# Kernel optimization log

Measured on AMD Instinct MI355X. Metric: run time of the kernel, lower is better.

Reference implementation:

```python
import jax, jax.numpy as jnp
import numpy as np

NUM_LEVELS = 3
NUM_STEPS = 4
STEP_SIZE = 2.0
MAX_ITER = 10
MOMENTUM = 0.1
D2R = np.array([np.pi / 180] * 3 + [1.0] * 3, dtype=np.float32)  # (6,) degree->rad for angles


def _rotmat(a):
    # a: (3,) rotation angles in radians; R = Rz @ Ry @ Rx
    cx, sx = jnp.cos(a[0]), jnp.sin(a[0])
    cy, sy = jnp.cos(a[1]), jnp.sin(a[1])
    cz, sz = jnp.cos(a[2]), jnp.sin(a[2])
    one = jnp.ones((), a.dtype)
    zero = jnp.zeros((), a.dtype)
    Rx = jnp.stack([jnp.stack([one, zero, zero]), jnp.stack([zero, cx, -sx]), jnp.stack([zero, sx, cx])])
    Ry = jnp.stack([jnp.stack([cy, zero, sy]), jnp.stack([zero, one, zero]), jnp.stack([-sy, zero, cy])])
    Rz = jnp.stack([jnp.stack([cz, -sz, zero]), jnp.stack([sz, cz, zero]), jnp.stack([zero, zero, one])])
    return Rz @ Ry @ Rx


def _warp_one(theta_deg, vol):
    # theta_deg: (6,) [rx,ry,rz in degrees, tx,ty,tz in normalized coords]; vol: (D,D,D)
    ang = theta_deg[:3] * jnp.float32(np.pi / 180)
    t = theta_deg[3:]
    R = _rotmat(ang)
    D = vol.shape[0]
    lin = jnp.linspace(-1.0, 1.0, D, dtype=vol.dtype)
    g0, g1, g2 = jnp.meshgrid(lin, lin, lin, indexing='ij')
    pts = jnp.stack([g0.ravel(), g1.ravel(), g2.ravel()])  # (3, D^3)
    p = R @ pts + t[:, None]
    idx = (p + 1.0) * ((D - 1) / 2.0)  # normalized [-1,1] -> voxel coords
    out = jax.scipy.ndimage.map_coordinates(vol, [idx[0], idx[1], idx[2]], order=1, mode='constant', cval=0.0)
    return out.reshape(D, D, D)


def _evaluate(theta_deg, src, tgt):
    # src/tgt: (B,1,D,D,D) -> per-sample mean MSE (loss(...).view(B,-1).mean(1))
    warped = jax.vmap(_warp_one)(theta_deg, src[:, 0])
    diff = (warped - tgt[:, 0]) ** 2
    return diff.reshape(diff.shape[0], -1).mean(1)


def _pool(x, f):
    # update_level: 2^level average-pool pyramid
    if f == 1:
        return x
    B, C, D = x.shape[0], x.shape[1], x.shape[2]
    return x.reshape(B, C, D // f, f, D // f, f, D // f, f).mean(axis=(3, 5, 7))


def _run_level(theta_deg, src, tgt, step_size0):
    # singlelevel(): num_steps outer steps, step_size halved each step,
    # each step runs max_iter masked GD iterations with FD gradients.
    B = theta_deg.shape[0]
    eye = jnp.eye(6, dtype=theta_deg.dtype)
    signed = jnp.concatenate([eye, -eye], axis=0)  # (12,6): +e_j rows then -e_j rows
    ev = lambda th: _evaluate(th, src, tgt)
    ev_fd = jax.vmap(ev)  # over the 12 FD perturbations

    buf = jnp.zeros_like(theta_deg)          # momentum buffer (created lazily in torch)
    has_buf = jnp.zeros((), bool)
    loss_all = jnp.zeros((B,), theta_deg.dtype)
    ss = step_size0
    for _ in range(NUM_STEPS):
        def body(i, state, ss=ss):
            theta, active, loss_all, buf, has_buf = state
            loss = ev(theta)
            lf = ev_fd(theta[None, :, :] + ss * signed[:, None, :])  # (12,B)
            grad = (lf[:6] - lf[6:]).T  # (B,6) undivided central differences (as in torch)
            loss_all = jnp.where(active, loss, loss_all)
            # gd_step with momentum: buf=grad on first call, else buf[active]=buf[active]*m+grad
            upd = jnp.where(has_buf, buf * MOMENTUM + grad, grad)
            buf = jnp.where(active[:, None], upd, buf)
            has_buf = jnp.ones((), bool)
            d = buf / (jnp.linalg.norm(buf, axis=-1, keepdims=True) + 1e-6)
            theta_try = theta + (-ss) * d
            loss_new = ev(theta_try)
            new_active = active & ((loss_new + 1e-4) < loss)  # shrinking active set
            theta = jnp.where(new_active[:, None], theta_try, theta)
            return theta, new_active, loss_all, buf, has_buf
        active = jnp.ones((B,), bool)
        theta_deg, active, loss_all, buf, has_buf = jax.lax.fori_loop(
            0, MAX_ITER, body, (theta_deg, active, loss_all, buf, has_buf))
        ss = ss / 2.0
    return theta_deg, loss_all


def _forward(theta, source, target):
    d2r = jnp.asarray(D2R)
    theta0 = theta
    # rad2degree(theta.detach())
    theta_deg = jax.lax.stop_gradient(theta / d2r)
    loss = jnp.zeros((theta.shape[0],), theta.dtype)
    for level in range(NUM_LEVELS - 1, -1, -1):
        f = 2 ** level
        theta_deg, loss = _run_level(theta_deg, _pool(source, f), _pool(target, f), STEP_SIZE * (2 ** level))
    # dtheta computed under no_grad; out = theta0 + dtheta
    dtheta = jax.lax.stop_gradient(theta_deg * d2r - theta0)
    return theta0 + dtheta, jax.lax.stop_gradient(loss)


def setup_inputs() -> dict:
    key = jax.random.key(0)
    k1, k2, k3 = jax.random.split(key, 3)
    B, D = 8, 64
    theta = jax.random.normal(k1, (B, 6), dtype=jnp.float32) * 0.05  # small initial misalignment (radians / normalized)
    source = jax.random.uniform(k2, (B, 1, D, D, D), dtype=jnp.float32)
    target = jax.random.uniform(k3, (B, 1, D, D, D), dtype=jnp.float32)
    return {"theta": theta, "source": source, "target": target}


def reference(theta, source, target):
    return _forward(theta, source, target)
```

## Files before the change

### kernel.cpp

```cpp
#include <hip/hip_runtime.h>

#define PI180F 0.017453292519943295f

__device__ __forceinline__ void compute_R(const float th[6], float R[9], float t[3]) {
    float ax = th[0] * PI180F, ay = th[1] * PI180F, az = th[2] * PI180F;
    float cx = cosf(ax), sx = sinf(ax);
    float cy = cosf(ay), sy = sinf(ay);
    float cz = cosf(az), sz = sinf(az);
    R[0] = cz * cy;  R[1] = (cz * sy) * sx - sz * cx;  R[2] = (cz * sy) * cx + sz * sx;
    R[3] = sz * cy;  R[4] = (sz * sy) * sx + cz * cx;  R[5] = (sz * sy) * cx - cz * sx;
    R[6] = -sy;      R[7] = cy * sx;                   R[8] = cy * cx;
    t[0] = th[3]; t[1] = th[4]; t[2] = th[5];
}

template<int D>
__device__ __forceinline__ float tri_sample_pad(const float* __restrict__ vol,
                                                float c0, float c1, float c2) {
    constexpr int P = D + 3;
    float f0 = floorf(c0), f1 = floorf(c1), f2 = floorf(c2);
    int i0 = (int)f0, i1 = (int)f1, i2 = (int)f2;
    float t0 = c0 - f0, t1 = c1 - f1, t2 = c2 - f2;
    float w0[2] = {1.0f - t0, t0};
    float w1[2] = {1.0f - t1, t1};
    float w2[2] = {1.0f - t2, t2};
    int ip0 = ((unsigned)(i0 + 1) <= (unsigned)D) ? (i0 + 1) : (D + 1);
    int ip1 = ((unsigned)(i1 + 1) <= (unsigned)D) ? (i1 + 1) : (D + 1);
    int ip2 = ((unsigned)(i2 + 1) <= (unsigned)D) ? (i2 + 1) : (D + 1);
    const float* p = vol + ((ip0 * P + ip1) * P + ip2);
    float acc = 0.0f;
    acc += ((w0[0] * w1[0]) * w2[0]) * p[0];
    acc += ((w0[0] * w1[0]) * w2[1]) * p[1];
    acc += ((w0[0] * w1[1]) * w2[0]) * p[P];
    acc += ((w0[0] * w1[1]) * w2[1]) * p[P + 1];
    acc += ((w0[1] * w1[0]) * w2[0]) * p[P * P];
    acc += ((w0[1] * w1[0]) * w2[1]) * p[P * P + 1];
    acc += ((w0[1] * w1[1]) * w2[0]) * p[P * P + P];
    acc += ((w0[1] * w1[1]) * w2[1]) * p[P * P + P + 1];
    return acc;
}

template<int D, int K>
__device__ __forceinline__ void eval_block(
    const float* __restrict__ srcp, const float* __restrict__ tgt,
    const float th[6], int b, int k, double* __restrict__ red)
{
    constexpr int logD = (D == 64) ? 6 : ((D == 32) ? 5 : 4);
    constexpr int n = D * D * D;
    constexpr int PS = (D + 3) * (D + 3) * (D + 3);
    float R[9], t[3];
    compute_R(th, R, t);

    constexpr int chunk = n / K;
    const int vstart = k * chunk;
    const float step = 2.0f / (float)(D - 1);
    const float scale = (float)(D - 1) * 0.5f;
    const float* s = srcp + (size_t)b * PS;
    const float* g = tgt + (size_t)b * n;

    double acc = 0.0;
    for (int v = vstart + threadIdx.x; v < vstart + chunk; v += 256) {
        int kk = v & (D - 1);
        int jj = (v >> logD) & (D - 1);
        int ii = v >> (2 * logD);
        float x0 = -1.0f + (float)ii * step;
        float x1 = -1.0f + (float)jj * step;
        float x2 = -1.0f + (float)kk * step;
        float p0 = R[0] * x0 + R[1] * x1 + R[2] * x2 + t[0];
        float p1 = R[3] * x0 + R[4] * x1 + R[5] * x2 + t[1];
        float p2 = R[6] * x0 + R[7] * x1 + R[8] * x2 + t[2];
        float c0 = (p0 + 1.0f) * scale;
        float c1 = (p1 + 1.0f) * scale;
        float c2 = (p2 + 1.0f) * scale;
        float w = tri_sample_pad<D>(s, c0, c1, c2);
        float d = w - g[v];
        acc += (double)(d * d);
    }

    red[threadIdx.x] = acc;
    __syncthreads();
#pragma unroll
    for (int st = 128; st > 0; st >>= 1) {
        if (threadIdx.x < st) red[threadIdx.x] += red[threadIdx.x + st];
        __syncthreads();
    }
}

template<int D, int K>
__global__ __launch_bounds__(256) void fd_kernel(
    const float* __restrict__ srcp, const float* __restrict__ tgt,
    const float* __restrict__ thetaIn, const float* __restrict__ lcurIn,
    const int* __restrict__ activeIn,
    float* __restrict__ thetaOut, float* __restrict__ lcurOut,
    int* __restrict__ activeOut,
    const float* __restrict__ ttry, const double* __restrict__ pB,
    double* __restrict__ partials,
    float ss, int first, int apply, int reset, int k3prev, int nprev)
{
    __shared__ double red[256];
    __shared__ float sth[6];
    __shared__ int sact;
    const int tid = threadIdx.x;
    const int gb = blockIdx.x;
    const int k = gb % K;
    const int e = gb / K;
    const int b = e & 7;
    const int c = first ? (e >> 3) : (e >> 3) + 1;

    if (apply) {
        if (tid < 32) {
            double v = (tid < k3prev) ? pB[b * k3prev + tid] : 0.0;
            v += __shfl_down(v, 16, 32);
            v += __shfl_down(v, 8, 32);
            v += __shfl_down(v, 4, 32);
            v += __shfl_down(v, 2, 32);
            v += __shfl_down(v, 1, 32);
            if (tid == 0) {
                int na = activeIn[b];
                float l = lcurIn[b];
                float th[6];
#pragma unroll
                for (int j = 0; j < 6; ++j) th[j] = thetaIn[b * 6 + j];
                if (na) {
                    float ln = (float)(v / (double)nprev);
                    if (ln + 1e-4f < l) {
#pragma unroll
                        for (int j = 0; j < 6; ++j) th[j] = ttry[b * 6 + j];
                        l = ln;
                    } else {
                        na = 0;
                    }
                }
                if (reset) na = 1;
#pragma unroll
                for (int j = 0; j < 6; ++j) sth[j] = th[j];
                sact = na;
                if (((e >> 3) == 0) && (k == 0)) {
#pragma unroll
                    for (int j = 0; j < 6; ++j) thetaOut[b * 6 + j] = th[j];
                    lcurOut[b] = l;
                    activeOut[b] = na;
                }
            }
        }
        __syncthreads();
    } else {
        if (tid < 6) sth[tid] = thetaIn[b * 6 + tid];
        if (tid == 0) sact = activeIn[b];
        __syncthreads();
    }

    if (!sact) return;
    float th[6];
#pragma unroll
    for (int j = 0; j < 6; ++j) th[j] = sth[j];
    if (c > 0) {
        int j = (c - 1) % 6;
        th[j] += (c <= 6) ? ss : -ss;
    }
    eval_block<D, K>(srcp, tgt, th, b, k, red);
    if (tid == 0) partials[(size_t)(c * 8 + b) * K + k] = red[0];
}

template<int D, int K3, int K>
__global__ __launch_bounds__(256) void trial_kernel(
    const float* __restrict__ srcp, const float* __restrict__ tgt,
    const float* __restrict__ theta, float* __restrict__ lcur,
    const int* __restrict__ active,
    const float* __restrict__ momIn, float* __restrict__ momOut,
    float* __restrict__ ttry, float* __restrict__ lall,
    const double* __restrict__ pA, double* __restrict__ pB,
    float ss, int first)
{
    constexpr int n = D * D * D;
    __shared__ double red[256];
    __shared__ float lossf[13];
    __shared__ float sttry[6];
    const int tid = threadIdx.x;
    const int gb = blockIdx.x;
    const int k = gb % K3;
    const int b = gb / K3;

    if (!active[b]) {
        if (k == 0 && tid < 6) momOut[b * 6 + tid] = momIn[b * 6 + tid];
        return;
    }

    const int nconf = first ? 13 : 12;
#pragma unroll
    for (int p = 0; p < 2; ++p) {
        int ci = p * 8 + (tid >> 5);
        if (ci < nconf) {
            int ca = first ? ci : ci + 1;
            int kk = tid & 31;
            double v = (kk < K) ? pA[(size_t)(ca * 8 + b) * K + kk] : 0.0;
            v += __shfl_down(v, 16, 32);
            v += __shfl_down(v, 8, 32);
            v += __shfl_down(v, 4, 32);
            v += __shfl_down(v, 2, 32);
            v += __shfl_down(v, 1, 32);
            if (kk == 0) lossf[ca] = (float)(v / (double)n);
        }
    }
    __syncthreads();
    if (tid == 0) {
        float lb = first ? lossf[0] : lcur[b];
        float ub[6];
#pragma unroll
        for (int j = 0; j < 6; ++j) {
            float grad = lossf[1 + j] - lossf[7 + j];
            float u = first ? grad : (momIn[b * 6 + j] * 0.1f + grad);
            ub[j] = u;
        }
        float ss2 = 0.0f;
#pragma unroll
        for (int j = 0; j < 6; ++j) ss2 += ub[j] * ub[j];
        float denom = sqrtf(ss2) + 1e-6f;
#pragma unroll
        for (int j = 0; j < 6; ++j) sttry[j] = theta[b * 6 + j] - ss * (ub[j] / denom);
        if (k == 0) {
            lall[b] = lb;
            if (first) lcur[b] = lb;
#pragma unroll
            for (int j = 0; j < 6; ++j) momOut[b * 6 + j] = ub[j];
#pragma unroll
            for (int j = 0; j < 6; ++j) ttry[b * 6 + j] = sttry[j];
        }
    }
    __syncthreads();
    float th[6];
#pragma unroll
    for (int j = 0; j < 6; ++j) th[j] = sttry[j];
    eval_block<D, K3>(srcp, tgt, th, b, k, red);
    if (tid == 0) pB[(size_t)b * K3 + k] = red[0];
}

__global__ __launch_bounds__(256) void finalize_kernel(
    const float* __restrict__ theta0,
    const float* __restrict__ theta, const float* __restrict__ lcur,
    const int* __restrict__ active, const float* __restrict__ ttry,
    const double* __restrict__ pB, const float* __restrict__ lall,
    float* __restrict__ out)
{
    __shared__ double rs[8];
    __shared__ float fth[48];
    const int tid = threadIdx.x;
    const int r = tid >> 5, l = tid & 31;
    {
        double v = pB[r * 32 + l];
        v += __shfl_down(v, 16, 32);
        v += __shfl_down(v, 8, 32);
        v += __shfl_down(v, 4, 32);
        v += __shfl_down(v, 2, 32);
        v += __shfl_down(v, 1, 32);
        if (l == 0) rs[r] = v;
    }
    __syncthreads();
    if (tid < 8) {
        int b = tid;
        bool acc = false;
        if (active[b]) {
            float ln = (float)(rs[b] / 262144.0);
            acc = (ln + 1e-4f < lcur[b]);
        }
        for (int j = 0; j < 6; ++j)
            fth[b * 6 + j] = acc ? ttry[b * 6 + j] : theta[b * 6 + j];
    }
    __syncthreads();
    if (tid < 48) {
        int j = tid % 6;
        float d2r = (j < 3) ? PI180F : 1.0f;
        float td = fth[tid] * d2r;
        out[tid] = theta0[tid] + (td - theta0[tid]);
    } else if (tid < 56) {
        out[tid] = lall[tid - 48];
    }
}

template<int f>
__global__ void pool_pad_kernel(const float* __restrict__ src, const float* __restrict__ tgt,
                                float* __restrict__ srcp, float* __restrict__ tgtp)
{
    constexpr int Do = 64 / f;
    constexpr int P = Do + 3;
    constexpr int n = 8 * Do * Do * Do;
    int idx = blockIdx.x * blockDim.x + threadIdx.x;
    if (idx >= 2 * n) return;
    bool is_src = idx < n;
    int id = is_src ? idx : idx - n;
    int kk = id % Do;
    int jj = (id / Do) % Do;
    int ii = (id / (Do * Do)) % Do;
    int b  = id / (Do * Do * Do);
    const float* v = (is_src ? src : tgt) + (size_t)b * 262144;
    double s = 0.0;
    for (int p = 0; p < f; ++p)
        for (int q = 0; q < f; ++q)
            for (int r = 0; r < f; ++r)
                s += (double)v[((ii * f + p) * 64 + (jj * f + q)) * 64 + (kk * f + r)];
    float val = (float)(s / (double)(f * f * f));
    if (is_src) srcp[(size_t)b * P * P * P + (((ii + 1) * P + (jj + 1)) * P + (kk + 1))] = val;
    else        tgtp[id] = val;
}

__global__ void pad_copy_kernel(const float* __restrict__ src, float* __restrict__ dst)
{
    int idx = blockIdx.x * blockDim.x + threadIdx.x;
    if (idx >= 8 * 262144) return;
    int kk = idx & 63;
    int jj = (idx >> 6) & 63;
    int ii = (idx >> 12) & 63;
    int b  = idx >> 18;
    dst[(size_t)b * 67 * 67 * 67 + (((ii + 1) * 67 + (jj + 1)) * 67 + (kk + 1))] = src[idx];
}

__global__ void init_kernel(const float* __restrict__ theta_in,
                            float* __restrict__ theta_deg,
                            float* __restrict__ lcur,
                            int* __restrict__ active)
{
    int t = threadIdx.x;
    if (t < 48) {
        int j = t % 6;
        float d2r = (j < 3) ? PI180F : 1.0f;
        theta_deg[t] = theta_in[t] / d2r;
    }
    if (t < 8) { active[t] = 1; lcur[t] = 0.0f; }
}

template<int D, int K, int K3>
static void run_level(const float* srcp, const float* tgt,
                      float* const thetaS[2], float* const lcurS[2], int* const activeS[2],
                      float* const momS[2], float* ttry, float* lall,
                      double* pA, double* pB,
                      int L, int& scur, int& mcur, int k3prevLvl, int nprevLvl,
                      float ss0, hipStream_t stream)
{
    float ssv = ss0;
    for (int s = 0; s < 4; ++s) {
        for (int it = 0; it < 10; ++it) {
            int first = (s == 0 && it == 0) ? 1 : 0;
            int apply = !(L == 0 && first);
            int reset = (it == 0) ? 1 : 0;
            int k3p = first ? k3prevLvl : K3;
            int np  = first ? nprevLvl  : D * D * D;
            int nconf = first ? 13 : 12;
            int so = apply ? (scur ^ 1) : scur;
            fd_kernel<D, K><<<nconf * 8 * K, 256, 0, stream>>>(
                srcp, tgt,
                thetaS[scur], lcurS[scur], activeS[scur],
                thetaS[so], lcurS[so], activeS[so],
                ttry, pB, pA, ssv, first, apply, reset, k3p, np);
            if (apply) scur ^= 1;
            trial_kernel<D, K3, K><<<8 * K3, 256, 0, stream>>>(
                srcp, tgt,
                thetaS[scur], lcurS[scur], activeS[scur],
                momS[mcur], momS[mcur ^ 1], ttry, lall, pA, pB, ssv, first);
            mcur ^= 1;
        }
        ssv *= 0.5f;
    }
}

extern "C" void kernel_launch(void* const* d_in, const int* in_sizes, int n_in,
                              void* d_out, int out_size, void* d_ws, size_t ws_size,
                              hipStream_t stream)
{
    const float* theta0 = (const float*)d_in[0];
    const float* source = (const float*)d_in[1];
    const float* target = (const float*)d_in[2];
    float* out = (float*)d_out;

    char* ws = (char*)d_ws;
    size_t off = 0;
    auto alloc = [&](size_t bytes) -> void* {
        off = (off + 255) & ~(size_t)255;
        void* p = ws + off;
        off += bytes;
        return p;
    };
    float* thetaS[2] = { (float*)alloc(48 * 4), (float*)alloc(48 * 4) };
    float* lcurS[2]  = { (float*)alloc(8 * 4),  (float*)alloc(8 * 4)  };
    int*   activeS[2]= { (int*)alloc(8 * 4),    (int*)alloc(8 * 4)    };
    float* momS[2]   = { (float*)alloc(48 * 4), (float*)alloc(48 * 4) };
    float* ttry  = (float*)alloc(48 * 4);
    float* lall  = (float*)alloc(8 * 4);
    double* pA   = (double*)alloc(13 * 8 * 32 * 8);
    double* pB   = (double*)alloc(8 * 32 * 8);
    float* tgt2  = (float*)alloc((size_t)8 * 32768 * 4);
    float* tgt4  = (float*)alloc((size_t)8 * 4096 * 4);
    const size_t PS16 = 19 * 19 * 19, PS32 = 35 * 35 * 35, PS64 = 67 * 67 * 67;
    float* pad16 = (float*)alloc((size_t)8 * PS16 * 4);
    float* pad32 = (float*)alloc((size_t)8 * PS32 * 4);
    float* pad64 = (float*)alloc((size_t)8 * PS64 * 4);

    hipMemsetAsync(pad16, 0, (size_t)8 * PS16 * 4, stream);
    hipMemsetAsync(pad32, 0, (size_t)8 * PS32 * 4, stream);
    hipMemsetAsync(pad64, 0, (size_t)8 * PS64 * 4, stream);

    pool_pad_kernel<2><<<(2 * 8 * 32768 + 255) / 256, 256, 0, stream>>>(source, target, pad32, tgt2);
    pool_pad_kernel<4><<<(2 * 8 * 4096 + 255) / 256, 256, 0, stream>>>(source, target, pad16, tgt4);
    pad_copy_kernel<<<(8 * 262144 + 255) / 256, 256, 0, stream>>>(source, pad64);
    init_kernel<<<1, 64, 0, stream>>>(theta0, thetaS[0], lcurS[0], activeS[0]);

    int scur = 0, mcur = 0;
    run_level<16,  2, 16>(pad16, tgt4,   thetaS, lcurS, activeS, momS, ttry, lall,
                          pA, pB, 0, scur, mcur, 16, 4096, 8.0f, stream);
    run_level<32,  8, 32>(pad32, tgt2,   thetaS, lcurS, activeS, momS, ttry, lall,
                          pA, pB, 1, scur, mcur, 16, 4096, 4.0f, stream);
    run_level<64, 32, 32>(pad64, target, thetaS, lcurS, activeS, momS, ttry, lall,
                          pA, pB, 2, scur, mcur, 32, 32768, 2.0f, stream);

    finalize_kernel<<<1, 256, 0, stream>>>(
        theta0, thetaS[scur], lcurS[scur], activeS[scur], ttry, pB, lall, out);
}
```

Measured before the change: 963.8 us.

## Restructure voxel loop by rows and raise trial split for level 64

The evaluation loop now assigns 16-thread groups to rows of the output grid. Each group computes the row-invariant part of the rotated coordinates once and reuses it across the row, which removes per-voxel index decoding and some multiply-adds. The level-64 trial kernel is split into 128 blocks per sample instead of 32, to use more of the GPU. The partial-sum reductions in the fd and finalize kernels now loop to handle more than 32 partials. Launch bounds now request 4 blocks per SM, which may limit registers and cause spills.

```diff
diff --git a/kernel.cpp b/kernel.cpp
--- a/kernel.cpp
+++ b/kernel.cpp
@@ -47,33 +47,48 @@
     constexpr int logD = (D == 64) ? 6 : ((D == 32) ? 5 : 4);
     constexpr int n = D * D * D;
     constexpr int PS = (D + 3) * (D + 3) * (D + 3);
+    constexpr int chunk = n / K;
+    constexpr int ROWS = chunk / D;
+    constexpr int NS = D / 16;
+    const float step = 2.0f / (float)(D - 1);
+    const float scale = (float)(D - 1) * 0.5f;
+
     float R[9], t[3];
     compute_R(th, R, t);
 
-    constexpr int chunk = n / K;
-    const int vstart = k * chunk;
-    const float step = 2.0f / (float)(D - 1);
-    const float scale = (float)(D - 1) * 0.5f;
     const float* s = srcp + (size_t)b * PS;
     const float* g = tgt + (size_t)b * n;
 
+    const int l15 = threadIdx.x & 15;
+    const int grp = threadIdx.x >> 4;
+    const int row0 = k * ROWS;
+
     double acc = 0.0;
-    for (int v = vstart + threadIdx.x; v < vstart + chunk; v += 256) {
-        int kk = v & (D - 1);
-        int jj = (v >> logD) & (D - 1);
-        int ii = v >> (2 * logD);
+#pragma unroll 2
+    for (int rit = 0; rit < ROWS / 16; ++rit) {
+        int row = row0 + rit * 16 + grp;
+        int ii = row >> logD;
+        int jj = row & (D - 1);
         float x0 = -1.0f + (float)ii * step;
         float x1 = -1.0f + (float)jj * step;
-        float x2 = -1.0f + (float)kk * step;
-        float p0 = R[0] * x0 + R[1] * x1 + R[2] * x2 + t[0];
-        float p1 = R[3] * x0 + R[4] * x1 + R[5] * x2 + t[1];
-        float p2 = R[6] * x0 + R[7] * x1 + R[8] * x2 + t[2];
-        float c0 = (p0 + 1.0f) * scale;
-        float c1 = (p1 + 1.0f) * scale;
-        float c2 = (p2 + 1.0f) * scale;
-        float w = tri_sample_pad<D>(s, c0, c1, c2);
-        float d = w - g[v];
-        acc += (double)(d * d);
+        float A0 = R[0] * x0 + R[1] * x1;
+        float A1 = R[3] * x0 + R[4] * x1;
+        float A2 = R[6] * x0 + R[7] * x1;
+        const float* grow = g + row * D;
+#pragma unroll
+        for (int si = 0; si < NS; ++si) {
+            int kk = l15 + si * 16;
+            float x2 = -1.0f + (float)kk * step;
+            float p0 = A0 + R[2] * x2 + t[0];
+            float p1 = A1 + R[5] * x2 + t[1];
+            float p2 = A2 + R[8] * x2 + t[2];
+            float c0 = (p0 + 1.0f) * scale;
+            float c1 = (p1 + 1.0f) * scale;
+            float c2 = (p2 + 1.0f) * scale;
+            float w = tri_sample_pad<D>(s, c0, c1, c2);
+            float d = w - grow[kk];
+            acc += (double)(d * d);
+        }
     }
 
     red[threadIdx.x] = acc;
@@ -86,7 +101,7 @@
 }
 
 template<int D, int K>
-__global__ __launch_bounds__(256) void fd_kernel(
+__global__ __launch_bounds__(256, 4) void fd_kernel(
     const float* __restrict__ srcp, const float* __restrict__ tgt,
     const float* __restrict__ thetaIn, const float* __restrict__ lcurIn,
     const int* __restrict__ activeIn,
@@ -108,7 +123,8 @@
 
     if (apply) {
         if (tid < 32) {
-            double v = (tid < k3prev) ? pB[b * k3prev + tid] : 0.0;
+            double v = 0.0;
+            for (int i = tid; i < k3prev; i += 32) v += pB[b * k3prev + i];
             v += __shfl_down(v, 16, 32);
             v += __shfl_down(v, 8, 32);
             v += __shfl_down(v, 4, 32);
@@ -162,7 +178,7 @@
 }
 
 template<int D, int K3, int K>
-__global__ __launch_bounds__(256) void trial_kernel(
+__global__ __launch_bounds__(256, 4) void trial_kernel(
     const float* __restrict__ srcp, const float* __restrict__ tgt,
     const float* __restrict__ theta, float* __restrict__ lcur,
     const int* __restrict__ active,
@@ -246,7 +262,8 @@
     const int tid = threadIdx.x;
     const int r = tid >> 5, l = tid & 31;
     {
-        double v = pB[r * 32 + l];
+        double v = 0.0;
+        for (int i = l; i < 128; i += 32) v += pB[r * 128 + i];
         v += __shfl_down(v, 16, 32);
         v += __shfl_down(v, 8, 32);
         v += __shfl_down(v, 4, 32);
@@ -385,7 +402,7 @@
     float* ttry  = (float*)alloc(48 * 4);
     float* lall  = (float*)alloc(8 * 4);
     double* pA   = (double*)alloc(13 * 8 * 32 * 8);
-    double* pB   = (double*)alloc(8 * 32 * 8);
+    double* pB   = (double*)alloc(8 * 128 * 8);
     float* tgt2  = (float*)alloc((size_t)8 * 32768 * 4);
     float* tgt4  = (float*)alloc((size_t)8 * 4096 * 4);
     const size_t PS16 = 19 * 19 * 19, PS32 = 35 * 35 * 35, PS64 = 67 * 67 * 67;
@@ -403,12 +420,12 @@
     init_kernel<<<1, 64, 0, stream>>>(theta0, thetaS[0], lcurS[0], activeS[0]);
 
     int scur = 0, mcur = 0;
-    run_level<16,  2, 16>(pad16, tgt4,   thetaS, lcurS, activeS, momS, ttry, lall,
-                          pA, pB, 0, scur, mcur, 16, 4096, 8.0f, stream);
-    run_level<32,  8, 32>(pad32, tgt2,   thetaS, lcurS, activeS, momS, ttry, lall,
-                          pA, pB, 1, scur, mcur, 16, 4096, 4.0f, stream);
-    run_level<64, 32, 32>(pad64, target, thetaS, lcurS, activeS, momS, ttry, lall,
-                          pA, pB, 2, scur, mcur, 32, 32768, 2.0f, stream);
+    run_level<16,  2,  16>(pad16, tgt4,   thetaS, lcurS, activeS, momS, ttry, lall,
+                           pA, pB, 0, scur, mcur, 16, 4096, 8.0f, stream);
+    run_level<32,  8,  32>(pad32, tgt2,   thetaS, lcurS, activeS, momS, ttry, lall,
+                           pA, pB, 1, scur, mcur, 16, 4096, 4.0f, stream);
+    run_level<64, 32, 128>(pad64, target, thetaS, lcurS, activeS, momS, ttry, lall,
+                           pA, pB, 2, scur, mcur, 32, 32768, 2.0f, stream);
 
     finalize_kernel<<<1, 256, 0, stream>>>(
         theta0, thetaS[scur], lcurS[scur], activeS[scur], ttry, pB, lall, out);
```

Result: slower. 1.005 ms (+4.2%).

## Fuse trial evaluation with next iteration's FD evaluation into one kernel

Applied to the files above, without the earlier changes.

Merges the separate finite-difference kernel and trial-step kernel into a single opt_kernel. Each launch now decides on the previous trial, computes the next trial point, and evaluates the 12 perturbed losses around it, plus the trial point itself as configuration 0. This roughly halves the number of dependent launches per iteration and removes their launch and serialization gaps. It also changes K per level, folds padding zero-fill into the pooling and copy kernels in place of the memsets, and double-buffers ttry and the partials. The cost is extra evaluations around a trial that may get rejected, and more complex state handling.

```diff
diff --git a/kernel.cpp b/kernel.cpp
--- a/kernel.cpp
+++ b/kernel.cpp
@@ -1,6 +1,11 @@
 #include <hip/hip_runtime.h>
 
 #define PI180F 0.017453292519943295f
+
+#define F_APPLY  1
+#define F_RESET  2
+#define F_UPD    4
+#define F_BASEC0 8
 
 __device__ __forceinline__ void compute_R(const float th[6], float R[9], float t[3]) {
     float ax = th[0] * PI180F, ay = th[1] * PI180F, az = th[2] * PI180F;
@@ -52,13 +57,14 @@
 
     constexpr int chunk = n / K;
     const int vstart = k * chunk;
+    const int vend = vstart + chunk;
     const float step = 2.0f / (float)(D - 1);
     const float scale = (float)(D - 1) * 0.5f;
     const float* s = srcp + (size_t)b * PS;
     const float* g = tgt + (size_t)b * n;
 
     double acc = 0.0;
-    for (int v = vstart + threadIdx.x; v < vstart + chunk; v += 256) {
+    for (int v = vstart + threadIdx.x; v < vend; v += 256) {
         int kk = v & (D - 1);
         int jj = (v >> logD) & (D - 1);
         int ii = v >> (2 * logD);
@@ -86,29 +92,38 @@
 }
 
 template<int D, int K>
-__global__ __launch_bounds__(256) void fd_kernel(
+__global__ __launch_bounds__(256) void opt_kernel(
     const float* __restrict__ srcp, const float* __restrict__ tgt,
     const float* __restrict__ thetaIn, const float* __restrict__ lcurIn,
     const int* __restrict__ activeIn,
     float* __restrict__ thetaOut, float* __restrict__ lcurOut,
     int* __restrict__ activeOut,
-    const float* __restrict__ ttry, const double* __restrict__ pB,
-    double* __restrict__ partials,
-    float ss, int first, int apply, int reset, int k3prev, int nprev)
-{
+    float* __restrict__ lcurW,
+    const float* __restrict__ momIn, float* __restrict__ momOut,
+    const float* __restrict__ ttryIn, float* __restrict__ ttryOut,
+    float* __restrict__ lall,
+    const double* __restrict__ pIn, double* __restrict__ pOut,
+    float ss, int cbase, int flags, int k3prev, int nprev)
+{
+    constexpr int n = D * D * D;
     __shared__ double red[256];
-    __shared__ float sth[6];
+    __shared__ float lossf[13];
+    __shared__ float sth[6], sttry[6];
+    __shared__ float slcur;
     __shared__ int sact;
+
     const int tid = threadIdx.x;
     const int gb = blockIdx.x;
     const int k = gb % K;
     const int e = gb / K;
     const int b = e & 7;
-    const int c = first ? (e >> 3) : (e >> 3) + 1;
-
-    if (apply) {
+    const int c = cbase + (e >> 3);
+    const bool desig = ((e >> 3) == 0) && (k == 0);
+
+    if (flags & F_APPLY) {
         if (tid < 32) {
-            double v = (tid < k3prev) ? pB[b * k3prev + tid] : 0.0;
+            double v = 0.0;
+            for (int i = tid; i < k3prev; i += 32) v += pIn[b * k3prev + i];
             v += __shfl_down(v, 16, 32);
             v += __shfl_down(v, 8, 32);
             v += __shfl_down(v, 4, 32);
@@ -124,17 +139,18 @@
                     float ln = (float)(v / (double)nprev);
                     if (ln + 1e-4f < l) {
 #pragma unroll
-                        for (int j = 0; j < 6; ++j) th[j] = ttry[b * 6 + j];
+                        for (int j = 0; j < 6; ++j) th[j] = ttryIn[b * 6 + j];
                         l = ln;
                     } else {
                         na = 0;
                     }
                 }
-                if (reset) na = 1;
+                if (flags & F_RESET) na = 1;
 #pragma unroll
                 for (int j = 0; j < 6; ++j) sth[j] = th[j];
                 sact = na;
-                if (((e >> 3) == 0) && (k == 0)) {
+                slcur = l;
+                if (desig) {
 #pragma unroll
                     for (int j = 0; j < 6; ++j) thetaOut[b * 6 + j] = th[j];
                     lcurOut[b] = l;
@@ -142,96 +158,74 @@
                 }
             }
         }
-        __syncthreads();
     } else {
         if (tid < 6) sth[tid] = thetaIn[b * 6 + tid];
-        if (tid == 0) sact = activeIn[b];
+        if (tid == 0) { sact = activeIn[b]; slcur = lcurIn[b]; }
+    }
+    __syncthreads();
+
+    if (flags & F_UPD) {
+        if (sact) {
+            const bool bc0 = (flags & F_BASEC0) != 0;
+            const int nsl = bc0 ? 13 : 12;
+#pragma unroll
+            for (int p = 0; p < 2; ++p) {
+                int ci = p * 8 + (tid >> 5);
+                if (ci < nsl) {
+                    int ca = bc0 ? ci : ci + 1;
+                    int kk = tid & 31;
+                    double v = 0.0;
+                    for (int i = kk; i < K; i += 32) v += pIn[(size_t)(ca * 8 + b) * K + i];
+                    v += __shfl_down(v, 16, 32);
+                    v += __shfl_down(v, 8, 32);
+                    v += __shfl_down(v, 4, 32);
+                    v += __shfl_down(v, 2, 32);
+                    v += __shfl_down(v, 1, 32);
+                    if (kk == 0) lossf[ca] = (float)(v / (double)n);
+                }
+            }
+            __syncthreads();
+            if (tid == 0) {
+                float lb = bc0 ? lossf[0] : slcur;
+                float ub[6];
+#pragma unroll
+                for (int j = 0; j < 6; ++j) {
+                    float grad = lossf[1 + j] - lossf[7 + j];
+                    float u = bc0 ? grad : (momIn[b * 6 + j] * 0.1f + grad);
+                    ub[j] = u;
+                }
+                float ss2 = 0.0f;
+#pragma unroll
+                for (int j = 0; j < 6; ++j) ss2 += ub[j] * ub[j];
+                float denom = sqrtf(ss2) + 1e-6f;
+#pragma unroll
+                for (int j = 0; j < 6; ++j) sttry[j] = sth[j] - ss * (ub[j] / denom);
+                if (desig) {
+                    lall[b] = lb;
+                    if (bc0) lcurW[b] = lb;
+#pragma unroll
+                    for (int j = 0; j < 6; ++j) momOut[b * 6 + j] = ub[j];
+#pragma unroll
+                    for (int j = 0; j < 6; ++j) ttryOut[b * 6 + j] = sttry[j];
+                }
+            }
+        } else {
+            if (desig && tid < 6) momOut[b * 6 + tid] = momIn[b * 6 + tid];
+        }
         __syncthreads();
     }
 
     if (!sact) return;
-    float th[6];
-#pragma unroll
-    for (int j = 0; j < 6; ++j) th[j] = sth[j];
+
+    float evth[6];
+#pragma unroll
+    for (int j = 0; j < 6; ++j) evth[j] = (flags & F_UPD) ? sttry[j] : sth[j];
     if (c > 0) {
         int j = (c - 1) % 6;
-        th[j] += (c <= 6) ? ss : -ss;
-    }
-    eval_block<D, K>(srcp, tgt, th, b, k, red);
-    if (tid == 0) partials[(size_t)(c * 8 + b) * K + k] = red[0];
-}
-
-template<int D, int K3, int K>
-__global__ __launch_bounds__(256) void trial_kernel(
-    const float* __restrict__ srcp, const float* __restrict__ tgt,
-    const float* __restrict__ theta, float* __restrict__ lcur,
-    const int* __restrict__ active,
-    const float* __restrict__ momIn, float* __restrict__ momOut,
-    float* __restrict__ ttry, float* __restrict__ lall,
-    const double* __restrict__ pA, double* __restrict__ pB,
-    float ss, int first)
-{
-    constexpr int n = D * D * D;
-    __shared__ double red[256];
-    __shared__ float lossf[13];
-    __shared__ float sttry[6];
-    const int tid = threadIdx.x;
-    const int gb = blockIdx.x;
-    const int k = gb % K3;
-    const int b = gb / K3;
-
-    if (!active[b]) {
-        if (k == 0 && tid < 6) momOut[b * 6 + tid] = momIn[b * 6 + tid];
-        return;
-    }
-
-    const int nconf = first ? 13 : 12;
-#pragma unroll
-    for (int p = 0; p < 2; ++p) {
-        int ci = p * 8 + (tid >> 5);
-        if (ci < nconf) {
-            int ca = first ? ci : ci + 1;
-            int kk = tid & 31;
-            double v = (kk < K) ? pA[(size_t)(ca * 8 + b) * K + kk] : 0.0;
-            v += __shfl_down(v, 16, 32);
-            v += __shfl_down(v, 8, 32);
-            v += __shfl_down(v, 4, 32);
-            v += __shfl_down(v, 2, 32);
-            v += __shfl_down(v, 1, 32);
-            if (kk == 0) lossf[ca] = (float)(v / (double)n);
-        }
-    }
-    __syncthreads();
-    if (tid == 0) {
-        float lb = first ? lossf[0] : lcur[b];
-        float ub[6];
-#pragma unroll
-        for (int j = 0; j < 6; ++j) {
-            float grad = lossf[1 + j] - lossf[7 + j];
-            float u = first ? grad : (momIn[b * 6 + j] * 0.1f + grad);
-            ub[j] = u;
-        }
-        float ss2 = 0.0f;
-#pragma unroll
-        for (int j = 0; j < 6; ++j) ss2 += ub[j] * ub[j];
-        float denom = sqrtf(ss2) + 1e-6f;
-#pragma unroll
-        for (int j = 0; j < 6; ++j) sttry[j] = theta[b * 6 + j] - ss * (ub[j] / denom);
-        if (k == 0) {
-            lall[b] = lb;
-            if (first) lcur[b] = lb;
-#pragma unroll
-            for (int j = 0; j < 6; ++j) momOut[b * 6 + j] = ub[j];
-#pragma unroll
-            for (int j = 0; j < 6; ++j) ttry[b * 6 + j] = sttry[j];
-        }
-    }
-    __syncthreads();
-    float th[6];
-#pragma unroll
-    for (int j = 0; j < 6; ++j) th[j] = sttry[j];
-    eval_block<D, K3>(srcp, tgt, th, b, k, red);
-    if (tid == 0) pB[(size_t)b * K3 + k] = red[0];
+        evth[j] += (c <= 6) ? ss : -ss;
+    }
+    eval_block<D, K>(srcp, tgt, evth, b, k, red);
+    if (tid == 0) pOut[(size_t)(c * 8 + b) * K + k] = red[0];
 }
 
 __global__ __launch_bounds__(256) void finalize_kernel(
@@ -282,35 +276,54 @@
 {
     constexpr int Do = 64 / f;
     constexpr int P = Do + 3;
-    constexpr int n = 8 * Do * Do * Do;
+    constexpr int nPad = 8 * P * P * P;
+    constexpr int nLin = 8 * Do * Do * Do;
     int idx = blockIdx.x * blockDim.x + threadIdx.x;
-    if (idx >= 2 * n) return;
-    bool is_src = idx < n;
-    int id = is_src ? idx : idx - n;
-    int kk = id % Do;
-    int jj = (id / Do) % Do;
-    int ii = (id / (Do * Do)) % Do;
-    int b  = id / (Do * Do * Do);
-    const float* v = (is_src ? src : tgt) + (size_t)b * 262144;
-    double s = 0.0;
-    for (int p = 0; p < f; ++p)
-        for (int q = 0; q < f; ++q)
-            for (int r = 0; r < f; ++r)
-                s += (double)v[((ii * f + p) * 64 + (jj * f + q)) * 64 + (kk * f + r)];
-    float val = (float)(s / (double)(f * f * f));
-    if (is_src) srcp[(size_t)b * P * P * P + (((ii + 1) * P + (jj + 1)) * P + (kk + 1))] = val;
-    else        tgtp[id] = val;
+    if (idx < nPad) {
+        int kk = idx % P;
+        int jj = (idx / P) % P;
+        int ii = (idx / (P * P)) % P;
+        int b  = idx / (P * P * P);
+        float val = 0.0f;
+        if (ii >= 1 && ii <= Do && jj >= 1 && jj <= Do && kk >= 1 && kk <= Do) {
+            const float* v = src + (size_t)b * 262144;
+            int i0 = ii - 1, j0 = jj - 1, k0 = kk - 1;
+            double s = 0.0;
+            for (int p = 0; p < f; ++p)
+                for (int q = 0; q < f; ++q)
+                    for (int r = 0; r < f; ++r)
+                        s += (double)v[((i0 * f + p) * 64 + (j0 * f + q)) * 64 + (k0 * f + r)];
+            val = (float)(s / (double)(f * f * f));
+        }
+        srcp[idx] = val;
+    } else if (idx < nPad + nLin) {
+        int id = idx - nPad;
+        int kk = id % Do;
+        int jj = (id / Do) % Do;
+        int ii = (id / (Do * Do)) % Do;
+        int b  = id / (Do * Do * Do);
+        const float* v = tgt + (size_t)b * 262144;
+        double s = 0.0;
+        for (int p = 0; p < f; ++p)
+            for (int q = 0; q < f; ++q)
+                for (int r = 0; r < f; ++r)
+                    s += (double)v[((ii * f + p) * 64 + (jj * f + q)) * 64 + (kk * f + r)];
+        tgtp[id] = (float)(s / (double)(f * f * f));
+    }
 }
 
 __global__ void pad_copy_kernel(const float* __restrict__ src, float* __restrict__ dst)
 {
     int idx = blockIdx.x * blockDim.x + threadIdx.x;
-    if (idx >= 8 * 262144) return;
-    int kk = idx & 63;
-    int jj = (idx >> 6) & 63;
-    int ii = (idx >> 12) & 63;
-    int b  = idx >> 18;
-    dst[(size_t)b * 67 * 67 * 67 + (((ii + 1) * 67 + (jj + 1)) * 67 + (kk + 1))] = src[idx];
+    if (idx >= 8 * 67 * 67 * 67) return;
+    int kk = idx % 67;
+    int jj = (idx / 67) % 67;
+    int ii = (idx / (67 * 67)) % 67;
+    int b  = idx / (67 * 67 * 67);
+    float v = 0.0f;
+    if (ii >= 1 && ii <= 64 && jj >= 1 && jj <= 64 && kk >= 1 && kk <= 64)
+        v = src[(((size_t)b * 64 + (ii - 1)) * 64 + (jj - 1)) * 64 + (kk - 1)];
+    dst[idx] = v;
 }
 
 __global__ void init_kernel(const float* __restrict__ theta_in,
@@ -327,35 +340,54 @@
     if (t < 8) { active[t] = 1; lcur[t] = 0.0f; }
 }
 
-template<int D, int K, int K3>
-static void run_level(const float* srcp, const float* tgt,
-                      float* const thetaS[2], float* const lcurS[2], int* const activeS[2],
-                      float* const momS[2], float* ttry, float* lall,
-                      double* pA, double* pB,
-                      int L, int& scur, int& mcur, int k3prevLvl, int nprevLvl,
-                      float ss0, hipStream_t stream)
-{
+struct Bufs {
+    float *thetaS[2], *lcurS[2], *momS[2], *ttryS[2];
+    int   *activeS[2];
+    float *lall;
+    double *P[2];
+};
+
+template<int D, int K>
+static void run_level(const float* srcp, const float* tgt, Bufs& bf,
+                      int& scur, int& mcur, int& tcur, int& pcur,
+                      int k3prevLvl, int nprevLvl, float ss0, bool veryFirst,
+                      hipStream_t stream)
+{
+    constexpr int n = D * D * D;
     float ssv = ss0;
     for (int s = 0; s < 4; ++s) {
-        for (int it = 0; it < 10; ++it) {
-            int first = (s == 0 && it == 0) ? 1 : 0;
-            int apply = !(L == 0 && first);
-            int reset = (it == 0) ? 1 : 0;
-            int k3p = first ? k3prevLvl : K3;
-            int np  = first ? nprevLvl  : D * D * D;
-            int nconf = first ? 13 : 12;
-            int so = apply ? (scur ^ 1) : scur;
-            fd_kernel<D, K><<<nconf * 8 * K, 256, 0, stream>>>(
+        {
+            int flags = F_RESET | ((veryFirst && s == 0) ? 0 : F_APPLY);
+            int cb    = (s == 0) ? 0 : 1;
+            int nconf = (s == 0) ? 13 : 12;
+            int k3p   = (s == 0) ? k3prevLvl : K;
+            int np    = (s == 0) ? nprevLvl  : n;
+            opt_kernel<D, K><<<nconf * 8 * K, 256, 0, stream>>>(
                 srcp, tgt,
-                thetaS[scur], lcurS[scur], activeS[scur],
-                thetaS[so], lcurS[so], activeS[so],
-                ttry, pB, pA, ssv, first, apply, reset, k3p, np);
-            if (apply) scur ^= 1;
-            trial_kernel<D, K3, K><<<8 * K3, 256, 0, stream>>>(
+                bf.thetaS[scur], bf.lcurS[scur], bf.activeS[scur],
+                bf.thetaS[scur ^ 1], bf.lcurS[scur ^ 1], bf.activeS[scur ^ 1],
+                bf.lcurS[scur],
+                bf.momS[mcur], bf.momS[mcur ^ 1],
+                bf.ttryS[tcur], bf.ttryS[tcur ^ 1],
+                bf.lall, bf.P[pcur], bf.P[pcur ^ 1],
+                ssv, cb, flags, k3p, np);
+            if (flags & F_APPLY) scur ^= 1;
+            pcur ^= 1;
+        }
+        for (int j = 1; j <= 10; ++j) {
+            int flags = F_UPD | ((j == 1) ? ((s == 0) ? F_BASEC0 : 0) : F_APPLY);
+            int nconf = (j == 10) ? 1 : 13;
+            opt_kernel<D, K><<<nconf * 8 * K, 256, 0, stream>>>(
                 srcp, tgt,
-                thetaS[scur], lcurS[scur], activeS[scur],
-                momS[mcur], momS[mcur ^ 1], ttry, lall, pA, pB, ssv, first);
-            mcur ^= 1;
+                bf.thetaS[scur], bf.lcurS[scur], bf.activeS[scur],
+                bf.thetaS[scur ^ 1], bf.lcurS[scur ^ 1], bf.activeS[scur ^ 1],
+                bf.lcurS[scur],
+                bf.momS[mcur], bf.momS[mcur ^ 1],
+                bf.ttryS[tcur], bf.ttryS[tcur ^ 1],
+                bf.lall, bf.P[pcur], bf.P[pcur ^ 1],
+                ssv, 0, flags, K, n);
+            if (flags & F_APPLY) scur ^= 1;
+            mcur ^= 1; tcur ^= 1; pcur ^= 1;
         }
         ssv *= 0.5f;
     }
@@ -378,14 +410,16 @@
         off += bytes;
         return p;
     };
-    float* thetaS[2] = { (float*)alloc(48 * 4), (float*)alloc(48 * 4) };
-    float* lcurS[2]  = { (float*)alloc(8 * 4),  (float*)alloc(8 * 4)  };
-    int*   activeS[2]= { (int*)alloc(8 * 4),    (int*)alloc(8 * 4)    };
-    float* momS[2]   = { (float*)alloc(48 * 4), (float*)alloc(48 * 4) };
-    float* ttry  = (float*)alloc(48 * 4);
-    float* lall  = (float*)alloc(8 * 4);
-    double* pA   = (double*)alloc(13 * 8 * 32 * 8);
-    double* pB   = (double*)alloc(8 * 32 * 8);
+    Bufs bf;
+    for (int i = 0; i < 2; ++i) {
+        bf.thetaS[i]  = (float*)alloc(48 * 4);
+        bf.lcurS[i]   = (float*)alloc(8 * 4);
+        bf.activeS[i] = (int*)alloc(8 * 4);
+        bf.momS[i]    = (float*)alloc(48 * 4);
+        bf.ttryS[i]   = (float*)alloc(48 * 4);
+        bf.P[i]       = (double*)alloc(13 * 8 * 32 * 8);
+    }
+    bf.lall = (float*)alloc(8 * 4);
     float* tgt2  = (float*)alloc((size_t)8 * 32768 * 4);
     float* tgt4  = (float*)alloc((size_t)8 * 4096 * 4);
     const size_t PS16 = 19 * 19 * 19, PS32 = 35 * 35 * 35, PS64 = 67 * 67 * 67;
@@ -393,23 +427,19 @@
     float* pad32 = (float*)alloc((size_t)8 * PS32 * 4);
     float* pad64 = (float*)alloc((size_t)8 * PS64 * 4);
 
-    hipMemsetAsync(pad16, 0, (size_t)8 * PS16 * 4, stream);
-    hipMemsetAsync(pad32, 0, (size_t)8 * PS32 * 4, stream);
-    hipMemsetAsync(pad64, 0, (size_t)8 * PS64 * 4, stream);
-
-    pool_pad_kernel<2><<<(2 * 8 * 32768 + 255) / 256, 256, 0, stream>>>(source, target, pad32, tgt2);
-    pool_pad_kernel<4><<<(2 * 8 * 4096 + 255) / 256, 256, 0, stream>>>(source, target, pad16, tgt4);
-    pad_copy_kernel<<<(8 * 262144 + 255) / 256, 256, 0, stream>>>(source, pad64);
-    init_kernel<<<1, 64, 0, stream>>>(theta0, thetaS[0], lcurS[0], activeS[0]);
-
-    int scur = 0, mcur = 0;
-    run_level<16,  2, 16>(pad16, tgt4,   thetaS, lcurS, activeS, momS, ttry, lall,
-                          pA, pB, 0, scur, mcur, 16, 4096, 8.0f, stream);
-    run_level<32,  8, 32>(pad32, tgt2,   thetaS, lcurS, activeS, momS, ttry, lall,
-                          pA, pB, 1, scur, mcur, 16, 4096, 4.0f, stream);
-    run_level<64, 32, 32>(pad64, target, thetaS, lcurS, activeS, momS, ttry, lall,
-                          pA, pB, 2, scur, mcur, 32, 32768, 2.0f, stream);
+    pool_pad_kernel<2><<<(int)((8 * PS32 + 8 * 32768 + 255) / 256), 256, 0, stream>>>(
+        source, target, pad32, tgt2);
+    pool_pad_kernel<4><<<(int)((8 * PS16 + 8 * 4096 + 255) / 256), 256, 0, stream>>>(
+        source, target, pad16, tgt4);
+    pad_copy_kernel<<<(int)((8 * PS64 + 255) / 256), 256, 0, stream>>>(source, pad64);
+    init_kernel<<<1, 64, 0, stream>>>(theta0, bf.thetaS[0], bf.lcurS[0], bf.activeS[0]);
+
+    int scur = 0, mcur = 0, tcur = 0, pcur = 0;
+    run_level<16,  8>(pad16, tgt4,   bf, scur, mcur, tcur, pcur,  1,     1, 8.0f, true,  stream);
+    run_level<32, 16>(pad32, tgt2,   bf, scur, mcur, tcur, pcur,  8,  4096, 4.0f, false, stream);
+    run_level<64, 32>(pad64, target, bf, scur, mcur, tcur, pcur, 16, 32768, 2.0f, false, stream);
 
     finalize_kernel<<<1, 256, 0, stream>>>(
-        theta0, thetaS[scur], lcurS[scur], activeS[scur], ttry, pB, lall, out);
-}
+        theta0, bf.thetaS[scur], bf.lcurS[scur], bf.activeS[scur],
+        bf.ttryS[tcur], bf.P[pcur], bf.lall, out);
+}
```

After: 977.3 us. No clear change (+1.4%).
